# Kernel optimization log

Measured on AMD Instinct MI355X. Metric: run time of the kernel, lower is better.

Reference implementation:

```python
import jax, jax.numpy as jnp
import numpy as np

B, S, D = 2, 1024, 4096
N_HEADS, KV_HEADS, HEAD_DIM = 32, 8, 128
EPS = 1e-6
ROPE_THETA = 1e6


def setup_inputs() -> dict:
    key = jax.random.key(0)
    ks = jax.random.split(key, 7)
    scale = 0.02
    x = jax.random.normal(ks[0], (B, S, D), dtype=jnp.float32)
    positions = jnp.broadcast_to(jnp.arange(S, dtype=jnp.int32)[None, :], (B, S))
    wq = jax.random.normal(ks[1], (D, N_HEADS, HEAD_DIM), dtype=jnp.float32) * scale
    wk = jax.random.normal(ks[2], (D, KV_HEADS, HEAD_DIM), dtype=jnp.float32) * scale
    wv = jax.random.normal(ks[3], (D, KV_HEADS, HEAD_DIM), dtype=jnp.float32) * scale
    wo = jax.random.normal(ks[4], (N_HEADS, HEAD_DIM, D), dtype=jnp.float32) * scale
    q_norm_w = 1.0 + jax.random.normal(ks[5], (HEAD_DIM,), dtype=jnp.float32) * 0.01
    k_norm_w = 1.0 + jax.random.normal(ks[6], (HEAD_DIM,), dtype=jnp.float32) * 0.01
    return {"x": x, "positions": positions, "wq": wq, "wk": wk, "wv": wv,
            "wo": wo, "q_norm_w": q_norm_w, "k_norm_w": k_norm_w}


def _rms_norm(t, w):
    # per-head RMSNorm over last (head_dim) axis
    var = jnp.mean(jnp.square(t), axis=-1, keepdims=True)
    return (t * jax.lax.rsqrt(var + EPS)) * w


def _rope(t, positions):
    # neox-style rotary embedding; t: [B, S, n, H], positions: [B, S]
    half = t.shape[-1] // 2
    inv_freq = 1.0 / (ROPE_THETA ** (jnp.arange(0, half, dtype=jnp.float32) / half))
    ang = positions.astype(jnp.float32)[..., None] * inv_freq  # [B, S, half]
    cos = jnp.cos(ang)[:, :, None, :]  # [B, S, 1, half]
    sin = jnp.sin(ang)[:, :, None, :]
    t1, t2 = t[..., :half], t[..., half:]
    return jnp.concatenate([t1 * cos - t2 * sin, t2 * cos + t1 * sin], axis=-1)


def reference(x, positions, wq, wk, wv, wo, q_norm_w, k_norm_w):
    # QKV projections (einsum layers: 'bsd,dnh->bsnh')
    q = jnp.einsum('bsd,dnh->bsnh', x, wq)  # [B, S, N, H]
    k = jnp.einsum('bsd,dkh->bskh', x, wk)  # [B, S, K, H]
    v = jnp.einsum('bsd,dkh->bskh', x, wv)
    # per-head QK RMSNorm, then RoPE
    q = _rope(_rms_norm(q, q_norm_w), positions)
    k = _rope(_rms_norm(k, k_norm_w), positions)
    # GQA: expand KV heads to query heads
    groups = N_HEADS // KV_HEADS
    k = jnp.repeat(k, groups, axis=2)  # [B, S, N, H]
    v = jnp.repeat(v, groups, axis=2)
    sm_scale = HEAD_DIM ** -0.5
    scores = jnp.einsum('bqnh,btnh->bnqt', q, k) * sm_scale  # [B, N, S, S]
    causal = jnp.tril(jnp.ones((S, S), dtype=bool))
    scores = jnp.where(causal[None, None], scores, jnp.finfo(scores.dtype).min)
    probs = jax.nn.softmax(scores, axis=-1)
    attn = jnp.einsum('bnqt,btnh->bqnh', probs, v)  # [B, S, N, H]
    out = jnp.einsum('bqnh,nhd->bqd', attn, wo)  # output projection
    return out
```

## Files before the change

### kernel.cpp

```cpp
#include <hip/hip_runtime.h>
#include <stdint.h>

#define S_LEN   1024
#define D_MODEL 4096
#define NHQ     32
#define NKV     8
#define HD      128
#define NTOK    2048
#define NQKV    6144
#define SM_SCALE 0.08838834764831843f

typedef __attribute__((ext_vector_type(8))) __bf16 bf16x8;
typedef __attribute__((ext_vector_type(4))) float f32x4;

__device__ __forceinline__ unsigned short f2bf(float f) {
  union { float f; unsigned u; } x; x.f = f;
  unsigned r = x.u + 0x7fffu + ((x.u >> 16) & 1u);
  return (unsigned short)(r >> 16);
}
__device__ __forceinline__ float bf2f(unsigned short u) {
  union { unsigned u; float f; } x; x.u = (unsigned)u << 16; return x.f;
}

__device__ __forceinline__ void gload_lds16(const void* g, void* l) {
  __builtin_amdgcn_global_load_lds((__attribute__((address_space(1))) void*)g,
                                   (__attribute__((address_space(3))) void*)l,
                                   16, 0, 0);
}

__global__ void k_f32_to_bf16(const float* __restrict__ in,
                              unsigned short* __restrict__ out, int n8) {
  int i = blockIdx.x * blockDim.x + threadIdx.x;
  if (i >= n8) return;
  const float4* p = (const float4*)(in + (size_t)i * 8);
  float4 v0 = p[0], v1 = p[1];
  uint4 o;
  o.x = f2bf(v0.x) | ((unsigned)f2bf(v0.y) << 16);
  o.y = f2bf(v0.z) | ((unsigned)f2bf(v0.w) << 16);
  o.z = f2bf(v1.x) | ((unsigned)f2bf(v1.y) << 16);
  o.w = f2bf(v1.z) | ((unsigned)f2bf(v1.w) << 16);
  *(uint4*)(out + (size_t)i * 8) = o;
}

__global__ void k_transpose(const float* __restrict__ in,
                            unsigned short* __restrict__ out, int R, int C) {
  __shared__ float t[32][33];
  int c = threadIdx.x & 31, r0 = threadIdx.x >> 5;
  int cb = blockIdx.x * 32, rb = blockIdx.y * 32;
#pragma unroll
  for (int i = 0; i < 4; ++i) {
    int r = r0 + i * 8;
    t[r][c] = in[(size_t)(rb + r) * C + cb + c];
  }
  __syncthreads();
#pragma unroll
  for (int i = 0; i < 4; ++i) {
    int r = r0 + i * 8;
    out[(size_t)(cb + r) * R + rb + c] = f2bf(t[c][r]);
  }
}


#define LGKM0 { asm volatile("s_waitcnt lgkmcnt(0)" ::: "memory"); \
                __builtin_amdgcn_sched_barrier(0); }
#define SCHED __builtin_amdgcn_sched_barrier(0);
#define BAR   __builtin_amdgcn_s_barrier();
#define GATE  { if constexpr (MH + NF / 2 == 4)                                 \
                  asm volatile("s_waitcnt vmcnt(4)" ::: "memory");              \
                else                                                            \
                  asm volatile("s_waitcnt vmcnt(3)" ::: "memory"); }

#define STGA(h, bufb, kOff)                                                     \
  _Pragma("unroll")                                                             \
  for (int i_ = 0; i_ < MH; ++i_)                                               \
    gload_lds16(gA[i_] + (kOff) + (h) * 64,                                     \
                smem + (bufb) + (h) * (MH * 8192) + dA[i_]);

#define STGB(h, bufb, kOff)                                                     \
  _Pragma("unroll")                                                             \
  for (int i_ = 0; i_ < NF / 2; ++i_)                                           \
    gload_lds16(gB[i_] + (kOff) + (h) * 64,                                     \
                smem + (bufb) + ABYTES + (h) * (NF * 4096) + dB[i_]);

#define RD_A(dst, mh, kh, bufb)                                                 \
  _Pragma("unroll")                                                             \
  for (int mf = 0; mf < 4; ++mf) {                                              \
    int row = wr * (MH * 64) + (mh) * 64 + mf * 16 + lr;                        \
    dst[mf] = *(const bf16x8*)(smem + (bufb) + (kh) * (MH * 8192) + row * 64    \
                               + ((lg * 16) ^ (((row >> 1) & 3) << 4)));        \
  }

#define RD_B(dst, kh, bufb)                                                     \
  _Pragma("unroll")                                                             \
  for (int nf = 0; nf < NF; ++nf) {                                             \
    int row = wc * (NF * 16) + nf * 16 + lr;                                    \
    dst[nf] = *(const bf16x8*)(smem + (bufb) + ABYTES + (kh) * (NF * 4096)      \
                               + row * 64 + ((lg * 16) ^ (((row >> 1) & 3) << 4))); \
  }

#define MFMA16(mh, AF, BF)                                                      \
  __builtin_amdgcn_s_setprio(1);                                                \
  _Pragma("unroll")                                                             \
  for (int mf = 0; mf < 4; ++mf)                                                \
    _Pragma("unroll")                                                           \
    for (int nf = 0; nf < NF; ++nf)                                             \
      acc[(mh) * 4 + mf][nf] = __builtin_amdgcn_mfma_f32_16x16x32_bf16(         \
          AF[mf], BF[nf], acc[(mh) * 4 + mf][nf], 0, 0, 0);                     \
  __builtin_amdgcn_s_setprio(0);

template <int MH, int NF, typename OutT>
__global__ __launch_bounds__(512, 1) void k_gemm256(
    const unsigned short* __restrict__ Aptr,
    const unsigned short* __restrict__ Bptr,
    OutT* __restrict__ C, int Kstride, int ldc, int NT, int SGN, int nxn) {
  extern __shared__ __align__(16) char smem[];
  constexpr int ABYTES = MH * 16384;
  constexpr int BUFST = MH * 16384 + NF * 8192;
  int tid = threadIdx.x;
  int l = tid & 63;
  int w = tid >> 6;
  int lr = l & 15, lg = l >> 4;
  int wr = w >> 2, wc = w & 3;
  int per_xcd = gridDim.x >> 3;
  int x8 = blockIdx.x & 7, i = blockIdx.x >> 3;
  int SGM = per_xcd / SGN;
  int xr = x8 / nxn, xc = x8 - xr * nxn;
  int iy = i / SGN;
  int by = xr * SGM + iy, bx = xc * SGN + (i - iy * SGN);
  int bm = by * (MH * 128), bn = bx * (NF * 64);

  const char* gA[MH]; int dA[MH];
#pragma unroll
  for (int i_ = 0; i_ < MH; ++i_) {
    int lin = i_ * 512 + tid;
    int r_ = lin >> 2, slot = lin & 3, sw = slot ^ ((r_ >> 1) & 3);
    gA[i_] = (const char*)(Aptr + (size_t)(bm + r_) * Kstride) + sw * 16;
    dA[i_] = lin * 16;
  }
  const char* gB[NF / 2]; int dB[NF / 2];
#pragma unroll
  for (int i_ = 0; i_ < NF / 2; ++i_) {
    int lin = i_ * 512 + tid;
    int r_ = lin >> 2, slot = lin & 3, sw = slot ^ ((r_ >> 1) & 3);
    gB[i_] = (const char*)(Bptr + (size_t)(bn + r_) * Kstride) + sw * 16;
    dB[i_] = lin * 16;
  }

  f32x4 acc[MH * 4][NF] = {};
  bf16x8 afA[4], afB[4], bfA[NF], bfB[NF];

  STGA(0, 0, 0) STGB(0, 0, 0)
  STGA(1, 0, 0) STGB(1, 0, 0)
  GATE
  BAR
  RD_A(afA, 0, 0, 0) RD_B(bfA, 0, 0)

  for (int kt = 0; kt < NT; ++kt) {
    int curb = (kt & 1) * BUFST;
    int nxtb = BUFST - curb;
    int kOff = (kt + 1) * 128;
    if constexpr (MH == 2) {
      STGA(0, nxtb, kOff)
      BAR LGKM0
      RD_A(afB, 1, 0, curb) SCHED
      MFMA16(0, afA, bfA)
      BAR
      STGB(0, nxtb, kOff)
      GATE BAR LGKM0
      RD_A(afA, 0, 1, curb) RD_B(bfB, 1, curb) SCHED
      MFMA16(1, afB, bfA)
      BAR
      STGA(1, nxtb, kOff)
      BAR LGKM0
      RD_A(afB, 1, 1, curb) SCHED
      MFMA16(0, afA, bfB)
      BAR
      STGB(1, nxtb, kOff)
      GATE BAR LGKM0
      RD_A(afA, 0, 0, nxtb) RD_B(bfA, 0, nxtb) SCHED
      MFMA16(1, afB, bfB)
      BAR
    } else {
      STGA(0, nxtb, kOff) STGB(0, nxtb, kOff)
      GATE BAR LGKM0
      RD_A(afB, 0, 1, curb) RD_B(bfB, 1, curb) SCHED
      MFMA16(0, afA, bfA)
      BAR
      STGA(1, nxtb, kOff) STGB(1, nxtb, kOff)
      GATE BAR LGKM0
      RD_A(afA, 0, 0, nxtb) RD_B(bfA, 0, nxtb) SCHED
      MFMA16(0, afB, bfB)
      BAR
    }
  }

#pragma unroll
  for (int mh = 0; mh < MH; ++mh)
#pragma unroll
    for (int mf = 0; mf < 4; ++mf)
#pragma unroll
      for (int nf = 0; nf < NF; ++nf)
#pragma unroll
        for (int j = 0; j < 4; ++j) {
          size_t idx = (size_t)(bm + wr * (MH * 64) + mh * 64 + mf * 16 + lg * 4 + j) * ldc +
                       bn + wc * (NF * 16) + nf * 16 + lr;
          float v = acc[mh * 4 + mf][nf][j];
          if constexpr (sizeof(OutT) == 2) C[idx] = f2bf(v);
          else C[idx] = v;
        }
}

__global__ void k_norm_rope(const unsigned short* __restrict__ qkv,
                            const float* __restrict__ w,
                            const int* __restrict__ positions,
                            unsigned short* __restrict__ out, int nheads, int colbase,
                            float oscale) {
  int wid = blockIdx.x * 4 + (threadIdx.x >> 6);
  int lane = threadIdx.x & 63;
  int token = wid / nheads, head = wid - token * nheads;
  const unsigned short* src = qkv + (size_t)token * NQKV + colbase + head * HD;
  float e0 = bf2f(src[lane]), e1 = bf2f(src[lane + 64]);
  float ss = e0 * e0 + e1 * e1;
#pragma unroll
  for (int m = 1; m < 64; m <<= 1) ss += __shfl_xor(ss, m, 64);
  float rs = rsqrtf(ss * (1.0f / 128.0f) + 1e-6f);
  float n0 = e0 * rs * w[lane], n1 = e1 * rs * w[lane + 64];
  int pos = positions[token];
  float invf = exp2f((float)lane * (-19.931568569324174f / 64.0f));
  float ang = (float)pos * invf;
  float sv, cv;
  sincosf(ang, &sv, &cv);
  float o0 = (n0 * cv - n1 * sv) * oscale;
  float o1 = (n1 * cv + n0 * sv) * oscale;
  int b = token >> 10, s = token & 1023;
  size_t ob = ((size_t)(b * nheads + head) * S_LEN + s) * HD;
  out[ob + lane] = f2bf(o0);
  out[ob + 64 + lane] = f2bf(o1);
}

__global__ void k_v_transpose(const unsigned short* __restrict__ qkv,
                              unsigned short* __restrict__ vt) {
  __shared__ unsigned short t[32][33];
  int slice = blockIdx.z;
  int b = slice >> 3, kh = slice & 7;
  const unsigned short* in = qkv + (size_t)(b * S_LEN) * NQKV + 5120 + kh * HD;
  unsigned short* out = vt + (size_t)slice * HD * S_LEN;
  int c = threadIdx.x & 31, r0 = threadIdx.x >> 5;
  int s0 = blockIdx.y * 32, d0 = blockIdx.x * 32;
#pragma unroll
  for (int i = 0; i < 4; ++i) {
    int r = r0 + i * 8;
    t[r][c] = in[(size_t)(s0 + r) * NQKV + d0 + c];
  }
  __syncthreads();
#pragma unroll
  for (int i = 0; i < 4; ++i) {
    int r = r0 + i * 8;
    out[(size_t)(d0 + r) * S_LEN + s0 + c] = t[c][r];
  }
}

__global__ __launch_bounds__(256) void k_attn(const unsigned short* __restrict__ qh,
                                              const unsigned short* __restrict__ kbuf,
                                              const unsigned short* __restrict__ vtbuf,
                                              unsigned short* __restrict__ attn_out) {
  __shared__ __align__(16) unsigned short k_lds[64 * 128];
  __shared__ __align__(16) unsigned short v_lds[128 * 64];
  __shared__ __align__(16) unsigned short p_lds[4][16 * 64];
  int b = blockIdx.z, h = blockIdx.y, bx = blockIdx.x;
  int khd = h >> 2;
  int tid = threadIdx.x, w = tid >> 6, l = tid & 63;
  int lr = l & 15, lg = l >> 4;
  const unsigned short* K = kbuf + (size_t)(b * NKV + khd) * S_LEN * HD;
  const unsigned short* VT = vtbuf + (size_t)(b * NKV + khd) * HD * S_LEN;
  char* klp = (char*)k_lds;
  char* vlp = (char*)v_lds;
  char* plp = (char*)p_lds[w];
  int swz = (lr & 7) << 4;

  for (int strip = 0; strip < 2; ++strip) {
    int qs = strip ? (15 - bx) : bx;
    int q0 = qs * 64;
    const unsigned short* Q = qh + ((size_t)(b * NHQ + h) * S_LEN + q0 + w * 16) * HD;
    bf16x8 qf[4];
#pragma unroll
    for (int kk = 0; kk < 4; ++kk)
      qf[kk] = *(const bf16x8*)&Q[(size_t)lr * HD + kk * 32 + lg * 8];

    f32x4 o[8] = {};
    float m_[4], l_[4];
#pragma unroll
    for (int j = 0; j < 4; ++j) { m_[j] = -1e30f; l_[j] = 0.0f; }

    int nt = qs + 1;
    for (int t = 0; t < nt; ++t) {
      int t0 = t * 64;
      __syncthreads();
#pragma unroll
      for (int it = 0; it < 4; ++it) {
        int db = (tid + it * 256) * 16;
        int kr = db >> 8, kc = db & 255;
        gload_lds16(K + (size_t)(t0 + kr) * HD + ((kc ^ ((kr & 7) << 4)) >> 1), klp + db);
        int vr = db >> 7, vc = db & 127;
        gload_lds16(VT + (size_t)vr * S_LEN + t0 + ((vc ^ ((vr & 7) << 4)) >> 1), vlp + db);
      }
      __syncthreads();

      f32x4 sc[4];
      __builtin_amdgcn_s_setprio(1);
#pragma unroll
      for (int ct = 0; ct < 4; ++ct) {
        f32x4 s = {};
        int row = ct * 16 + lr;
#pragma unroll
        for (int kk = 0; kk < 4; ++kk) {
          bf16x8 kf = *(const bf16x8*)(klp + row * 256 + ((kk * 64 + lg * 16) ^ swz));
          s = __builtin_amdgcn_mfma_f32_16x16x32_bf16(qf[kk], kf, s, 0, 0, 0);
        }
        sc[ct] = s;
      }
      __builtin_amdgcn_s_setprio(0);

      bool full = (t < qs);
      float alpha[4];
#pragma unroll
      for (int j = 0; j < 4; ++j) {
        if (!full) {
          int rg = q0 + w * 16 + lg * 4 + j;
#pragma unroll
          for (int ct = 0; ct < 4; ++ct)
            sc[ct][j] = (t0 + ct * 16 + lr <= rg) ? sc[ct][j] : -1e30f;
        }
        float mx = fmaxf(fmaxf(sc[0][j], sc[1][j]), fmaxf(sc[2][j], sc[3][j]));
#pragma unroll
        for (int msk = 1; msk < 16; msk <<= 1) mx = fmaxf(mx, __shfl_xor(mx, msk, 64));
        float mn = fmaxf(m_[j], mx);
        alpha[j] = __expf(m_[j] - mn);
        int q = lg * 4 + j;
        int psw = (q & 7) << 4;
        float ps = 0.0f;
#pragma unroll
        for (int ct = 0; ct < 4; ++ct) {
          float p = __expf(sc[ct][j] - mn);
          ps += p;
          *(unsigned short*)(plp + q * 128 + (((ct * 16 + lr) * 2) ^ psw)) = f2bf(p);
        }
#pragma unroll
        for (int msk = 1; msk < 16; msk <<= 1) ps += __shfl_xor(ps, msk, 64);
        l_[j] = l_[j] * alpha[j] + ps;
        m_[j] = mn;
      }
#pragma unroll
      for (int dc = 0; dc < 8; ++dc) {
        o[dc][0] *= alpha[0]; o[dc][1] *= alpha[1];
        o[dc][2] *= alpha[2]; o[dc][3] *= alpha[3];
      }
      asm volatile("s_waitcnt lgkmcnt(0)" ::: "memory");
      __builtin_amdgcn_s_setprio(1);
#pragma unroll
      for (int kt = 0; kt < 2; ++kt) {
        bf16x8 pa = *(const bf16x8*)(plp + lr * 128 + ((kt * 64 + lg * 16) ^ swz));
#pragma unroll
        for (int dc = 0; dc < 8; ++dc) {
          int vrow = dc * 16 + lr;
          bf16x8 vf = *(const bf16x8*)(vlp + vrow * 128 + ((kt * 64 + lg * 16) ^ swz));
          o[dc] = __builtin_amdgcn_mfma_f32_16x16x32_bf16(pa, vf, o[dc], 0, 0, 0);
        }
      }
      __builtin_amdgcn_s_setprio(0);
    }

#pragma unroll
    for (int j = 0; j < 4; ++j) {
      int rg = q0 + w * 16 + lg * 4 + j;
      size_t row = (size_t)(b * S_LEN + rg) * D_MODEL + h * HD;
      float inv = 1.0f / l_[j];
#pragma unroll
      for (int dc = 0; dc < 8; ++dc)
        attn_out[row + dc * 16 + lr] = f2bf(o[dc][j] * inv);
    }
  }
}

extern "C" void kernel_launch(void* const* d_in, const int* in_sizes, int n_in,
                              void* d_out, int out_size, void* d_ws, size_t ws_size,
                              hipStream_t stream) {
  const float* x        = (const float*)d_in[0];
  const int* positions  = (const int*)d_in[1];
  const float* wq       = (const float*)d_in[2];
  const float* wk       = (const float*)d_in[3];
  const float* wv       = (const float*)d_in[4];
  const float* wo       = (const float*)d_in[5];
  const float* qnw      = (const float*)d_in[6];
  const float* knw      = (const float*)d_in[7];
  float* out            = (float*)d_out;

  char* ws = (char*)d_ws;
  unsigned short* xb   = (unsigned short*)(ws);
  unsigned short* wB   = (unsigned short*)(ws + 16777216);
  unsigned short* woT  = (unsigned short*)(ws + 67108864);
  unsigned short* qkvb = (unsigned short*)(ws + 100663296);
  unsigned short* qh   = wB;
  unsigned short* khb  = (unsigned short*)(ws + 33554432);
  unsigned short* vtb  = (unsigned short*)(ws + 37748736);
  unsigned short* attn = xb;

  dim3 tb(256);
  k_f32_to_bf16<<<4096, tb, 0, stream>>>(x, xb, 1048576);
  k_transpose<<<dim3(128, 128), tb, 0, stream>>>(wq, wB, 4096, 4096);
  k_transpose<<<dim3(32, 128), tb, 0, stream>>>(wk, wB + (size_t)4096 * 4096, 4096, 1024);
  k_transpose<<<dim3(32, 128), tb, 0, stream>>>(wv, wB + (size_t)5120 * 4096, 4096, 1024);
  k_transpose<<<dim3(128, 128), tb, 0, stream>>>(wo, woT, 4096, 4096);

  k_gemm256<2, 4, unsigned short><<<dim3(192), dim3(512), 131072, stream>>>(
      xb, wB, qkvb, 4096, 6144, 64, 6, 4);

  k_norm_rope<<<16384, tb, 0, stream>>>(qkvb, qnw, positions, qh, 32, 0, SM_SCALE);
  k_norm_rope<<<4096, tb, 0, stream>>>(qkvb, knw, positions, khb, 8, 4096, 1.0f);
  k_v_transpose<<<dim3(4, 32, 16), tb, 0, stream>>>(qkvb, vtb);

  k_attn<<<dim3(8, 32, 2), tb, 0, stream>>>(qh, khb, vtb, attn);

  k_gemm256<1, 4, float><<<dim3(256), dim3(512), 98304, stream>>>(
      attn, woT, out, 4096, 4096, 64, 4, 4);
}
```

Measured before the change: 329.8 us.

## Split-K the output projection into 256-row tiles and widen weight transpose

```diff
diff --git a/kernel.cpp b/kernel.cpp
--- a/kernel.cpp
+++ b/kernel.cpp
@@ -42,21 +42,29 @@
   *(uint4*)(out + (size_t)i * 8) = o;
 }
 
-__global__ void k_transpose(const float* __restrict__ in,
-                            unsigned short* __restrict__ out, int R, int C) {
-  __shared__ float t[32][33];
-  int c = threadIdx.x & 31, r0 = threadIdx.x >> 5;
-  int cb = blockIdx.x * 32, rb = blockIdx.y * 32;
+__global__ __launch_bounds__(256) void k_transpose64(const float* __restrict__ in,
+                                                     unsigned short* __restrict__ out,
+                                                     int R, int C) {
+  __shared__ float t[64][65];
+  int rb = blockIdx.y * 64, cb = blockIdx.x * 64;
+  int c4 = (threadIdx.x & 15) * 4;
+  int r0 = threadIdx.x >> 4;
 #pragma unroll
   for (int i = 0; i < 4; ++i) {
-    int r = r0 + i * 8;
-    t[r][c] = in[(size_t)(rb + r) * C + cb + c];
+    int r = r0 + i * 16;
+    float4 v = *(const float4*)&in[(size_t)(rb + r) * C + cb + c4];
+    t[r][c4] = v.x; t[r][c4 + 1] = v.y; t[r][c4 + 2] = v.z; t[r][c4 + 3] = v.w;
   }
   __syncthreads();
+  int rg = (threadIdx.x & 15) * 4;
+  int cc0 = threadIdx.x >> 4;
 #pragma unroll
   for (int i = 0; i < 4; ++i) {
-    int r = r0 + i * 8;
-    out[(size_t)(cb + r) * R + rb + c] = f2bf(t[c][r]);
+    int cc = cc0 + i * 16;
+    ushort4 u;
+    u.x = f2bf(t[rg][cc]);     u.y = f2bf(t[rg + 1][cc]);
+    u.z = f2bf(t[rg + 2][cc]); u.w = f2bf(t[rg + 3][cc]);
+    *(ushort4*)&out[(size_t)(cb + cc) * R + rb + rg] = u;
   }
 }
 
@@ -65,28 +73,25 @@
                 __builtin_amdgcn_sched_barrier(0); }
 #define SCHED __builtin_amdgcn_sched_barrier(0);
 #define BAR   __builtin_amdgcn_s_barrier();
-#define GATE  { if constexpr (MH + NF / 2 == 4)                                 \
-                  asm volatile("s_waitcnt vmcnt(4)" ::: "memory");              \
-                else                                                            \
-                  asm volatile("s_waitcnt vmcnt(3)" ::: "memory"); }
+#define GATE  asm volatile("s_waitcnt vmcnt(4)" ::: "memory");
 
 #define STGA(h, bufb, kOff)                                                     \
   _Pragma("unroll")                                                             \
-  for (int i_ = 0; i_ < MH; ++i_)                                               \
+  for (int i_ = 0; i_ < 2; ++i_)                                                \
     gload_lds16(gA[i_] + (kOff) + (h) * 64,                                     \
-                smem + (bufb) + (h) * (MH * 8192) + dA[i_]);
+                smem + (bufb) + (h) * 16384 + dA[i_]);
 
 #define STGB(h, bufb, kOff)                                                     \
   _Pragma("unroll")                                                             \
   for (int i_ = 0; i_ < NF / 2; ++i_)                                           \
     gload_lds16(gB[i_] + (kOff) + (h) * 64,                                     \
-                smem + (bufb) + ABYTES + (h) * (NF * 4096) + dB[i_]);
+                smem + (bufb) + 32768 + (h) * (NF * 4096) + dB[i_]);
 
 #define RD_A(dst, mh, kh, bufb)                                                 \
   _Pragma("unroll")                                                             \
   for (int mf = 0; mf < 4; ++mf) {                                              \
-    int row = wr * (MH * 64) + (mh) * 64 + mf * 16 + lr;                        \
-    dst[mf] = *(const bf16x8*)(smem + (bufb) + (kh) * (MH * 8192) + row * 64    \
+    int row = wr * 128 + (mh) * 64 + mf * 16 + lr;                              \
+    dst[mf] = *(const bf16x8*)(smem + (bufb) + (kh) * 16384 + row * 64          \
                                + ((lg * 16) ^ (((row >> 1) & 3) << 4)));        \
   }
 
@@ -94,7 +99,7 @@
   _Pragma("unroll")                                                             \
   for (int nf = 0; nf < NF; ++nf) {                                             \
     int row = wc * (NF * 16) + nf * 16 + lr;                                    \
-    dst[nf] = *(const bf16x8*)(smem + (bufb) + ABYTES + (kh) * (NF * 4096)      \
+    dst[nf] = *(const bf16x8*)(smem + (bufb) + 32768 + (kh) * (NF * 4096)       \
                                + row * 64 + ((lg * 16) ^ (((row >> 1) & 3) << 4))); \
   }
 
@@ -108,33 +113,36 @@
           AF[mf], BF[nf], acc[(mh) * 4 + mf][nf], 0, 0, 0);                     \
   __builtin_amdgcn_s_setprio(0);
 
-template <int MH, int NF, typename OutT>
+template <int NF, typename OutT>
 __global__ __launch_bounds__(512, 1) void k_gemm256(
     const unsigned short* __restrict__ Aptr,
     const unsigned short* __restrict__ Bptr,
-    OutT* __restrict__ C, int Kstride, int ldc, int NT, int SGN, int nxn) {
+    OutT* __restrict__ C, float* __restrict__ Cpart,
+    int Kstride, int ldc, int NT, int SGN, int nxn, int nps) {
   extern __shared__ __align__(16) char smem[];
-  constexpr int ABYTES = MH * 16384;
-  constexpr int BUFST = MH * 16384 + NF * 8192;
+  constexpr int BUFST = 32768 + NF * 8192;
   int tid = threadIdx.x;
   int l = tid & 63;
   int w = tid >> 6;
   int lr = l & 15, lg = l >> 4;
   int wr = w >> 2, wc = w & 3;
-  int per_xcd = gridDim.x >> 3;
-  int x8 = blockIdx.x & 7, i = blockIdx.x >> 3;
+  int ks = (blockIdx.x >= nps) ? 1 : 0;
+  int bid = blockIdx.x - ks * nps;
+  int per_xcd = nps >> 3;
+  int x8 = bid & 7, i = bid >> 3;
   int SGM = per_xcd / SGN;
   int xr = x8 / nxn, xc = x8 - xr * nxn;
   int iy = i / SGN;
   int by = xr * SGM + iy, bx = xc * SGN + (i - iy * SGN);
-  int bm = by * (MH * 128), bn = bx * (NF * 64);
-
-  const char* gA[MH]; int dA[MH];
-#pragma unroll
-  for (int i_ = 0; i_ < MH; ++i_) {
+  int bm = by * 256, bn = bx * (NF * 64);
+  int k0e = ks * NT * 64;
+
+  const char* gA[2]; int dA[2];
+#pragma unroll
+  for (int i_ = 0; i_ < 2; ++i_) {
     int lin = i_ * 512 + tid;
     int r_ = lin >> 2, slot = lin & 3, sw = slot ^ ((r_ >> 1) & 3);
-    gA[i_] = (const char*)(Aptr + (size_t)(bm + r_) * Kstride) + sw * 16;
+    gA[i_] = (const char*)(Aptr + (size_t)(bm + r_) * Kstride + k0e) + sw * 16;
     dA[i_] = lin * 16;
   }
   const char* gB[NF / 2]; int dB[NF / 2];
@@ -142,11 +150,11 @@
   for (int i_ = 0; i_ < NF / 2; ++i_) {
     int lin = i_ * 512 + tid;
     int r_ = lin >> 2, slot = lin & 3, sw = slot ^ ((r_ >> 1) & 3);
-    gB[i_] = (const char*)(Bptr + (size_t)(bn + r_) * Kstride) + sw * 16;
+    gB[i_] = (const char*)(Bptr + (size_t)(bn + r_) * Kstride + k0e) + sw * 16;
     dB[i_] = lin * 16;
   }
 
-  f32x4 acc[MH * 4][NF] = {};
+  f32x4 acc[8][NF] = {};
   bf16x8 afA[4], afB[4], bfA[NF], bfB[NF];
 
   STGA(0, 0, 0) STGB(0, 0, 0)
@@ -159,55 +167,55 @@
     int curb = (kt & 1) * BUFST;
     int nxtb = BUFST - curb;
     int kOff = (kt + 1) * 128;
-    if constexpr (MH == 2) {
-      STGA(0, nxtb, kOff)
-      BAR LGKM0
-      RD_A(afB, 1, 0, curb) SCHED
-      MFMA16(0, afA, bfA)
-      BAR
-      STGB(0, nxtb, kOff)
-      GATE BAR LGKM0
-      RD_A(afA, 0, 1, curb) RD_B(bfB, 1, curb) SCHED
-      MFMA16(1, afB, bfA)
-      BAR
-      STGA(1, nxtb, kOff)
-      BAR LGKM0
-      RD_A(afB, 1, 1, curb) SCHED
-      MFMA16(0, afA, bfB)
-      BAR
-      STGB(1, nxtb, kOff)
-      GATE BAR LGKM0
-      RD_A(afA, 0, 0, nxtb) RD_B(bfA, 0, nxtb) SCHED
-      MFMA16(1, afB, bfB)
-      BAR
-    } else {
-      STGA(0, nxtb, kOff) STGB(0, nxtb, kOff)
-      GATE BAR LGKM0
-      RD_A(afB, 0, 1, curb) RD_B(bfB, 1, curb) SCHED
-      MFMA16(0, afA, bfA)
-      BAR
-      STGA(1, nxtb, kOff) STGB(1, nxtb, kOff)
-      GATE BAR LGKM0
-      RD_A(afA, 0, 0, nxtb) RD_B(bfA, 0, nxtb) SCHED
-      MFMA16(0, afB, bfB)
-      BAR
-    }
-  }
-
-#pragma unroll
-  for (int mh = 0; mh < MH; ++mh)
+    STGA(0, nxtb, kOff)
+    BAR LGKM0
+    RD_A(afB, 1, 0, curb) SCHED
+    MFMA16(0, afA, bfA)
+    BAR
+    STGB(0, nxtb, kOff)
+    GATE BAR LGKM0
+    RD_A(afA, 0, 1, curb) RD_B(bfB, 1, curb) SCHED
+    MFMA16(1, afB, bfA)
+    BAR
+    STGA(1, nxtb, kOff)
+    BAR LGKM0
+    RD_A(afB, 1, 1, curb) SCHED
+    MFMA16(0, afA, bfB)
+    BAR
+    STGB(1, nxtb, kOff)
+    GATE BAR LGKM0
+    RD_A(afA, 0, 0, nxtb) RD_B(bfA, 0, nxtb) SCHED
+    MFMA16(1, afB, bfB)
+    BAR
+  }
+
+#pragma unroll
+  for (int mh = 0; mh < 2; ++mh)
 #pragma unroll
     for (int mf = 0; mf < 4; ++mf)
 #pragma unroll
       for (int nf = 0; nf < NF; ++nf)
 #pragma unroll
         for (int j = 0; j < 4; ++j) {
-          size_t idx = (size_t)(bm + wr * (MH * 64) + mh * 64 + mf * 16 + lg * 4 + j) * ldc +
+          size_t idx = (size_t)(bm + wr * 128 + mh * 64 + mf * 16 + lg * 4 + j) * ldc +
                        bn + wc * (NF * 16) + nf * 16 + lr;
           float v = acc[mh * 4 + mf][nf][j];
-          if constexpr (sizeof(OutT) == 2) C[idx] = f2bf(v);
+          if (ks) Cpart[idx] = v;
+          else if constexpr (sizeof(OutT) == 2) C[idx] = f2bf(v);
           else C[idx] = v;
         }
+}
+
+__global__ void k_reduce_add(float* __restrict__ out, const float* __restrict__ p,
+                             int n4) {
+  int i = blockIdx.x * blockDim.x + threadIdx.x;
+  int stride = gridDim.x * blockDim.x;
+  for (; i < n4; i += stride) {
+    float4 a = ((const float4*)out)[i];
+    float4 b = ((const float4*)p)[i];
+    a.x += b.x; a.y += b.y; a.z += b.z; a.w += b.w;
+    ((float4*)out)[i] = a;
+  }
 }
 
 __global__ void k_norm_rope(const unsigned short* __restrict__ qkv,
@@ -404,16 +412,17 @@
   unsigned short* khb  = (unsigned short*)(ws + 33554432);
   unsigned short* vtb  = (unsigned short*)(ws + 37748736);
   unsigned short* attn = xb;
+  float*          part = (float*)(ws + 16777216);
 
   dim3 tb(256);
   k_f32_to_bf16<<<4096, tb, 0, stream>>>(x, xb, 1048576);
-  k_transpose<<<dim3(128, 128), tb, 0, stream>>>(wq, wB, 4096, 4096);
-  k_transpose<<<dim3(32, 128), tb, 0, stream>>>(wk, wB + (size_t)4096 * 4096, 4096, 1024);
-  k_transpose<<<dim3(32, 128), tb, 0, stream>>>(wv, wB + (size_t)5120 * 4096, 4096, 1024);
-  k_transpose<<<dim3(128, 128), tb, 0, stream>>>(wo, woT, 4096, 4096);
-
-  k_gemm256<2, 4, unsigned short><<<dim3(192), dim3(512), 131072, stream>>>(
-      xb, wB, qkvb, 4096, 6144, 64, 6, 4);
+  k_transpose64<<<dim3(64, 64), tb, 0, stream>>>(wq, wB, 4096, 4096);
+  k_transpose64<<<dim3(16, 64), tb, 0, stream>>>(wk, wB + (size_t)4096 * 4096, 4096, 1024);
+  k_transpose64<<<dim3(16, 64), tb, 0, stream>>>(wv, wB + (size_t)5120 * 4096, 4096, 1024);
+  k_transpose64<<<dim3(64, 64), tb, 0, stream>>>(wo, woT, 4096, 4096);
+
+  k_gemm256<4, unsigned short><<<dim3(192), dim3(512), 131072, stream>>>(
+      xb, wB, qkvb, nullptr, 4096, 6144, 64, 6, 4, 192);
 
   k_norm_rope<<<16384, tb, 0, stream>>>(qkvb, qnw, positions, qh, 32, 0, SM_SCALE);
   k_norm_rope<<<4096, tb, 0, stream>>>(qkvb, knw, positions, khb, 8, 4096, 1.0f);
@@ -421,6 +430,7 @@
 
   k_attn<<<dim3(8, 32, 2), tb, 0, stream>>>(qh, khb, vtb, attn);
 
-  k_gemm256<1, 4, float><<<dim3(256), dim3(512), 98304, stream>>>(
-      attn, woT, out, 4096, 4096, 64, 4, 4);
-}
+  k_gemm256<4, float><<<dim3(256), dim3(512), 131072, stream>>>(
+      attn, woT, out, part, 4096, 4096, 32, 4, 4, 128);
+  k_reduce_add<<<2048, tb, 0, stream>>>(out, part, 2097152);
+}
```

Measured after the change: 337.8 us. +2.4%, slower.
